# Kernel optimization log

Hardware: AMD Instinct MI355X
Metric: run time of the kernel (lower is better)

The kernel has to match this reference:

```python
import jax, jax.numpy as jnp
import numpy as np

B, N, M, K = 2, 50000, 50000, 16
C_IN, C_ADD, C_MID = 64, 3, 16


def setup_inputs() -> dict:
    key = jax.random.key(0)
    k1, k2, k3, k4 = jax.random.split(key, 4)
    return {
        "input_features": jax.random.normal(k1, (B, N, C_IN), dtype=jnp.float32),
        "neighbor_inds": jax.random.randint(k2, (B, M, K), 0, N, dtype=jnp.int64),
        "weightnet": jax.random.normal(k3, (B, M, K, C_MID), dtype=jnp.float32),
        "additional_features": jax.random.normal(k4, (B, M, K, C_ADD), dtype=jnp.float32),
    }


def reference(input_features, neighbor_inds, weightnet, additional_features):
    # Gather neighbor features: [B, M, K, C_in]
    gathered = jax.vmap(lambda feat, idx: feat[idx])(input_features, neighbor_inds)
    # Concatenate additional per-neighbor features: [B, M, K, C_in + C_add]
    cat = jnp.concatenate([gathered, additional_features], axis=-1)
    # Weighted reduce over neighbors: [B, M, C_total, C_mid]
    out = jnp.einsum("bmkc,bmkw->bmcw", cat, weightnet)
    b, m = out.shape[:2]
    return out.reshape(b, m, -1)
```

## Files before the change

### kernel.cpp

```cpp
#include <hip/hip_runtime.h>
#include <cstdint>
#include <cstddef>


namespace {
constexpr int B_   = 2;
constexpr int N_   = 50000;
constexpr int M_   = 50000;
constexpr int KNB  = 16;
constexpr int CIN  = 64;
constexpr int COUT = 67 * 16;
constexpr int PAIRS = B_ * M_;
constexpr int FELEMS = B_ * N_ * CIN;
}

typedef unsigned int u32;
typedef float  f32x4   __attribute__((ext_vector_type(4)));
typedef short  short8  __attribute__((ext_vector_type(8)));
typedef short  short4v __attribute__((ext_vector_type(4)));
typedef u32    u32x4   __attribute__((ext_vector_type(4)));
typedef u32    u32x2   __attribute__((ext_vector_type(2)));

struct IdxS   { int v[16]; };
struct StageF { float bg[4][8]; float ad[8]; float wf[8]; };

static __device__ __forceinline__ short8 pack_bf8(const float* x) {
  u32x4 w;
  #pragma unroll
  for (int q = 0; q < 4; ++q)
    w[q] = __builtin_amdgcn_perm(__builtin_bit_cast(u32, x[2*q+1]),
                                 __builtin_bit_cast(u32, x[2*q]),
                                 0x07060302u);
  return __builtin_bit_cast(short8, w);
}

static __device__ __forceinline__ short4v pack_bf4(const float* x) {
  u32x2 w;
  #pragma unroll
  for (int q = 0; q < 2; ++q)
    w[q] = __builtin_amdgcn_perm(__builtin_bit_cast(u32, x[2*q+1]),
                                 __builtin_bit_cast(u32, x[2*q]),
                                 0x07060302u);
  return __builtin_bit_cast(short4v, w);
}

static __device__ __forceinline__ u32 bfrne(float x) {
  u32 u = __builtin_bit_cast(u32, x);
  return (u + 0x7FFFu + ((u >> 16) & 1u)) >> 16;
}

__global__ __launch_bounds__(256)
void cvt_feat_bf16(const float* __restrict__ src, unsigned short* __restrict__ dst) {
  const int n4 = FELEMS / 4;
  int i = blockIdx.x * blockDim.x + threadIdx.x;
  const int stride = gridDim.x * blockDim.x;
  const f32x4* s4 = reinterpret_cast<const f32x4*>(src);
  for (; i < n4; i += stride) {
    f32x4 v = s4[i];
    u32x2 w;
    w[0] = bfrne(v[0]) | (bfrne(v[1]) << 16);
    w[1] = bfrne(v[2]) | (bfrne(v[3]) << 16);
    *reinterpret_cast<u32x2*>(dst + 4 * (size_t)i) = w;
  }
}

static __device__ __forceinline__ void load_idx(const int* __restrict__ idxp, IdxS& r) {
  #pragma unroll
  for (int j = 0; j < 16; ++j)
    r.v[j] = __builtin_amdgcn_readfirstlane(idxp[j]);
}

#if __has_builtin(__builtin_amdgcn_mfma_f32_16x16x16bf16_1k)

__global__ __launch_bounds__(256, 8)
void pconv10(const unsigned short* __restrict__ tbl, const int* __restrict__ inds,
             const float* __restrict__ wnet, const float* __restrict__ addf,
             float* __restrict__ out)
{
  const int lane = threadIdx.x & 63;
  const int cc = lane & 15, g = lane >> 4;
  const int g1 = g & 1, g2 = g >> 1;
  const int gw = __builtin_amdgcn_readfirstlane(
      (int)((blockIdx.x * blockDim.x + threadIdx.x) >> 6));
  const int nw = (int)((gridDim.x * blockDim.x) >> 6);
  if (gw >= PAIRS) return;

  IdxS iCur, iNext;
  load_idx(inds + (size_t)gw * KNB, iCur);

  for (int p = gw; p < PAIRS; p += nw) {
    const int pn = (p + nw < PAIRS) ? (p + nw) : gw;
    load_idx(inds + (size_t)pn * KNB, iNext);

    const int b = (p >= M_) ? 1 : 0;
    const unsigned short* __restrict__ fb  = tbl + (size_t)b * N_ * CIN;
    const float* __restrict__ wnp = wnet + (size_t)p * 256;
    const float* __restrict__ adp = addf + (size_t)p * 48;

    int row[4];
    #pragma unroll
    for (int j = 0; j < 4; ++j) {
      const int ra = g1 ? iCur.v[4 + j]  : iCur.v[j];
      const int rb = g1 ? iCur.v[12 + j] : iCur.v[8 + j];
      row[j] = g2 ? rb : ra;
    }

    u32 bg[4][4];
    #pragma unroll
    for (int j = 0; j < 4; ++j) {
      const unsigned short* __restrict__ rp = fb + (((u32)row[j]) << 6) + (u32)cc;
      #pragma unroll
      for (int t = 0; t < 4; ++t)
        bg[t][j] = rp[t * 16];
    }

    float wf[4];
    const float* __restrict__ wp = wnp + g * 64 + cc;
    #pragma unroll
    for (int j = 0; j < 4; ++j)
      wf[j] = __builtin_nontemporal_load(wp + j * 16);

    float ad[4];
    const float* __restrict__ ap = adp + g * 12 + cc;
    #pragma unroll
    for (int j = 0; j < 4; ++j)
      ad[j] = (cc < 3) ? __builtin_nontemporal_load(ap + j * 3) : 0.f;

    const short4v a = pack_bf4(wf);
    float* __restrict__ op = out + (size_t)p * COUT;
    const int soff = cc * 16 + g * 4;

    #pragma unroll
    for (int t = 0; t < 4; ++t) {
      u32x2 w;
      w[0] = bg[t][0] | (bg[t][1] << 16);
      w[1] = bg[t][2] | (bg[t][3] << 16);
      const short4v bb = __builtin_bit_cast(short4v, w);
      f32x4 acc = {0.f, 0.f, 0.f, 0.f};
      acc = __builtin_amdgcn_mfma_f32_16x16x16bf16_1k(a, bb, acc, 0, 0, 0);
      __builtin_nontemporal_store(acc, reinterpret_cast<f32x4*>(op + soff + t * 256));
    }
    {
      const short4v bb = pack_bf4(ad);
      f32x4 acc = {0.f, 0.f, 0.f, 0.f};
      acc = __builtin_amdgcn_mfma_f32_16x16x16bf16_1k(a, bb, acc, 0, 0, 0);
      if (cc < 3)
        __builtin_nontemporal_store(acc, reinterpret_cast<f32x4*>(op + soff + 1024));
    }

    #pragma unroll
    for (int j = 0; j < 16; ++j) iCur.v[j] = iNext.v[j];
  }
}

#else

struct StageT { unsigned short bg[4][8]; float ad[8]; float wf[8]; };

static __device__ __forceinline__ void load_stage_t(const unsigned short* __restrict__ fb,
                                                    const float* __restrict__ wnp,
                                                    const float* __restrict__ adp,
                                                    const IdxS& I, int lane, StageT& S) {
  const int cc = lane & 15;
  if (lane < 32) {
    const int hi = lane >> 4;
    int rows[8];
    #pragma unroll
    for (int j = 0; j < 8; ++j) rows[j] = hi ? I.v[j + 8] : I.v[j];
    #pragma unroll
    for (int j = 0; j < 8; ++j) {
      const u32 rb = ((u32)rows[j]) << 6;
      #pragma unroll
      for (int t = 0; t < 4; ++t)
        S.bg[t][j] = fb[rb + (u32)(t * 16 + cc)];
    }
    const u32 woff = (hi ? 128u : 0u) + (u32)cc;
    #pragma unroll
    for (int j = 0; j < 8; ++j)
      S.wf[j] = __builtin_nontemporal_load(wnp + woff + j * 16);
    if (cc < 3) {
      const u32 aoff = (hi ? 24u : 0u) + (u32)cc;
      #pragma unroll
      for (int j = 0; j < 8; ++j)
        S.ad[j] = __builtin_nontemporal_load(adp + aoff + j * 3);
    }
  }
}

__global__ __launch_bounds__(256, 4)
void pconv10(const unsigned short* __restrict__ tbl, const int* __restrict__ inds,
             const float* __restrict__ wnet, const float* __restrict__ addf,
             float* __restrict__ out)
{
  const int lane = threadIdx.x & 63;
  const int gw = __builtin_amdgcn_readfirstlane(
      (int)((blockIdx.x * blockDim.x + threadIdx.x) >> 6));
  const int nw = (int)((gridDim.x * blockDim.x) >> 6);
  if (gw >= PAIRS) return;

  IdxS iCur, iNext;
  load_idx(inds + (size_t)gw * KNB, iCur);
  for (int p = gw; p < PAIRS; p += nw) {
    const int pn = (p + nw < PAIRS) ? (p + nw) : gw;
    load_idx(inds + (size_t)pn * KNB, iNext);
    const int b = (p >= M_) ? 1 : 0;
    StageT S = {};
    load_stage_t(tbl + (size_t)b * N_ * CIN, wnet + (size_t)p * 256,
                 addf + (size_t)p * 48, iCur, lane, S);
    const int cc = lane & 15, g = lane >> 4;
    const int soff = cc * 16 + g * 4;
    float* op = out + (size_t)p * COUT;
    const short8 a = pack_bf8(S.wf);
    #pragma unroll
    for (int t = 0; t < 4; ++t) {
      short8 bb;
      #pragma unroll
      for (int j = 0; j < 8; ++j) bb[j] = (short)S.bg[t][j];
      f32x4 acc = {0.f, 0.f, 0.f, 0.f};
      acc = __builtin_amdgcn_mfma_f32_16x16x32_bf16(a, bb, acc, 0, 0, 0);
      __builtin_nontemporal_store(acc, reinterpret_cast<f32x4*>(op + soff + t * 256));
    }
    {
      const short8 bb = pack_bf8(S.ad);
      f32x4 acc = {0.f, 0.f, 0.f, 0.f};
      acc = __builtin_amdgcn_mfma_f32_16x16x32_bf16(a, bb, acc, 0, 0, 0);
      if (cc < 3)
        __builtin_nontemporal_store(acc, reinterpret_cast<f32x4*>(op + soff + 1024));
    }
    #pragma unroll
    for (int j = 0; j < 16; ++j) iCur.v[j] = iNext.v[j];
  }
}

#endif

static __device__ __forceinline__ void load_stage_f(const float* __restrict__ fb,
                                                    const float* __restrict__ wnp,
                                                    const float* __restrict__ adp,
                                                    const IdxS& I, int lane, StageF& S) {
  const int cc = lane & 15;
  if (lane < 32) {
    const int hi = lane >> 4;
    int rows[8];
    #pragma unroll
    for (int j = 0; j < 8; ++j) rows[j] = hi ? I.v[j + 8] : I.v[j];
    #pragma unroll
    for (int j = 0; j < 8; ++j) {
      const u32 rb = ((u32)rows[j]) << 6;
      #pragma unroll
      for (int t = 0; t < 4; ++t)
        S.bg[t][j] = fb[rb + (u32)(t * 16 + cc)];
    }
    const u32 woff = (hi ? 128u : 0u) + (u32)cc;
    #pragma unroll
    for (int j = 0; j < 8; ++j)
      S.wf[j] = __builtin_nontemporal_load(wnp + woff + j * 16);
    if (cc < 3) {
      const u32 aoff = (hi ? 24u : 0u) + (u32)cc;
      #pragma unroll
      for (int j = 0; j < 8; ++j)
        S.ad[j] = __builtin_nontemporal_load(adp + aoff + j * 3);
    }
  }
}

__global__ __launch_bounds__(256, 4)
void pconv10_f32(const float* __restrict__ feat, const int* __restrict__ inds,
                 const float* __restrict__ wnet, const float* __restrict__ addf,
                 float* __restrict__ out)
{
  const int lane = threadIdx.x & 63;
  const int gw = __builtin_amdgcn_readfirstlane(
      (int)((blockIdx.x * blockDim.x + threadIdx.x) >> 6));
  const int nw = (int)((gridDim.x * blockDim.x) >> 6);
  if (gw >= PAIRS) return;

  IdxS iCur, iNext;
  load_idx(inds + (size_t)gw * KNB, iCur);
  for (int p = gw; p < PAIRS; p += nw) {
    const int pn = (p + nw < PAIRS) ? (p + nw) : gw;
    load_idx(inds + (size_t)pn * KNB, iNext);
    const int b = (p >= M_) ? 1 : 0;
    StageF S = {};
    load_stage_f(feat + (size_t)b * N_ * CIN, wnet + (size_t)p * 256,
                 addf + (size_t)p * 48, iCur, lane, S);
    const int cc = lane & 15, g = lane >> 4;
    const int soff = cc * 16 + g * 4;
    float* op = out + (size_t)p * COUT;
    const short8 a = pack_bf8(S.wf);
    #pragma unroll
    for (int t = 0; t < 4; ++t) {
      const short8 bb = pack_bf8(S.bg[t]);
      f32x4 acc = {0.f, 0.f, 0.f, 0.f};
      acc = __builtin_amdgcn_mfma_f32_16x16x32_bf16(a, bb, acc, 0, 0, 0);
      __builtin_nontemporal_store(acc, reinterpret_cast<f32x4*>(op + soff + t * 256));
    }
    {
      const short8 bb = pack_bf8(S.ad);
      f32x4 acc = {0.f, 0.f, 0.f, 0.f};
      acc = __builtin_amdgcn_mfma_f32_16x16x32_bf16(a, bb, acc, 0, 0, 0);
      if (cc < 3)
        __builtin_nontemporal_store(acc, reinterpret_cast<f32x4*>(op + soff + 1024));
    }
    #pragma unroll
    for (int j = 0; j < 16; ++j) iCur.v[j] = iNext.v[j];
  }
}

extern "C" void kernel_launch(void* const* d_in, const int* in_sizes, int n_in,
                              void* d_out, int out_size, void* d_ws, size_t ws_size,
                              hipStream_t stream) {
  const float* feat = (const float*)d_in[0];
  const int*   inds = (const int*)d_in[1];
  const float* wnet = (const float*)d_in[2];
  const float* addf = (const float*)d_in[3];
  float* outp = (float*)d_out;

  const size_t TBL_BYTES = (size_t)FELEMS * sizeof(unsigned short);

  dim3 grid(4096), block(256);
  if (ws_size >= TBL_BYTES) {
    unsigned short* tbl = (unsigned short*)d_ws;
    hipLaunchKernelGGL(cvt_feat_bf16, dim3(2048), dim3(256), 0, stream, feat, tbl);
    hipLaunchKernelGGL(pconv10, grid, block, 0, stream, tbl, inds, wnet, addf, outp);
  } else {
    hipLaunchKernelGGL(pconv10_f32, grid, block, 0, stream,
                       feat, inds, wnet, addf, outp);
  }
}
```

Before: 166.1 us.

## Software-pipeline gathers three pairs deep with rotating register stages

Restructures the MFMA path so each wave keeps three rotating stage buffers: the gathered feature rows, weightnet and additional loads for pair p+2 are issued while pair p is computed and stored, and the indices for p+3 are prefetched. The aim is to hide gather latency behind compute by keeping more memory requests in flight per wave. The cost is higher register use, so launch bounds drop from 8 to 4 waves per SIMD, which reduces occupancy. The loop is unrolled three times with a break in each copy.

```diff
diff --git a/kernel.cpp b/kernel.cpp
--- a/kernel.cpp
+++ b/kernel.cpp
@@ -22,6 +22,7 @@
 typedef u32    u32x2   __attribute__((ext_vector_type(2)));
 
 struct IdxS   { int v[16]; };
+struct StageG { u32 bg[4][4]; float wf[4]; float ad[4]; };
 struct StageF { float bg[4][8]; float ad[8]; float wf[8]; };
 
 static __device__ __forceinline__ short8 pack_bf8(const float* x) {
@@ -72,8 +73,67 @@
 
 #if __has_builtin(__builtin_amdgcn_mfma_f32_16x16x16bf16_1k)
 
-__global__ __launch_bounds__(256, 8)
-void pconv10(const unsigned short* __restrict__ tbl, const int* __restrict__ inds,
+static __device__ __forceinline__ void issue_loads(const unsigned short* __restrict__ tbl,
+                                                   const float* __restrict__ wnet,
+                                                   const float* __restrict__ addf,
+                                                   int q, const IdxS& I,
+                                                   int cc, int g1, int g2, int g,
+                                                   StageG& S) {
+  const unsigned short* __restrict__ fb =
+      tbl + ((q >= M_) ? (size_t)N_ * CIN : 0);
+  const float* __restrict__ wnp = wnet + (size_t)q * 256;
+  const float* __restrict__ adp = addf + (size_t)q * 48;
+
+  int row[4];
+  #pragma unroll
+  for (int j = 0; j < 4; ++j) {
+    const int ra = g1 ? I.v[4 + j]  : I.v[j];
+    const int rb = g1 ? I.v[12 + j] : I.v[8 + j];
+    row[j] = g2 ? rb : ra;
+  }
+  #pragma unroll
+  for (int j = 0; j < 4; ++j) {
+    const unsigned short* __restrict__ rp = fb + (((u32)row[j]) << 6) + (u32)cc;
+    #pragma unroll
+    for (int t = 0; t < 4; ++t)
+      S.bg[t][j] = rp[t * 16];
+  }
+  const float* __restrict__ wp = wnp + g * 64 + cc;
+  #pragma unroll
+  for (int j = 0; j < 4; ++j)
+    S.wf[j] = __builtin_nontemporal_load(wp + j * 16);
+  const float* __restrict__ ap = adp + g * 12 + cc;
+  #pragma unroll
+  for (int j = 0; j < 4; ++j)
+    S.ad[j] = (cc < 3) ? __builtin_nontemporal_load(ap + j * 3) : 0.f;
+}
+
+static __device__ __forceinline__ void compute_store(const StageG& S,
+                                                     float* __restrict__ op,
+                                                     int cc, int g) {
+  const int soff = cc * 16 + g * 4;
+  const short4v a = pack_bf4(S.wf);
+  #pragma unroll
+  for (int t = 0; t < 4; ++t) {
+    u32x2 w;
+    w[0] = S.bg[t][0] | (S.bg[t][1] << 16);
+    w[1] = S.bg[t][2] | (S.bg[t][3] << 16);
+    const short4v bb = __builtin_bit_cast(short4v, w);
+    f32x4 acc = {0.f, 0.f, 0.f, 0.f};
+    acc = __builtin_amdgcn_mfma_f32_16x16x16bf16_1k(a, bb, acc, 0, 0, 0);
+    __builtin_nontemporal_store(acc, reinterpret_cast<f32x4*>(op + soff + t * 256));
+  }
+  {
+    const short4v bb = pack_bf4(S.ad);
+    f32x4 acc = {0.f, 0.f, 0.f, 0.f};
+    acc = __builtin_amdgcn_mfma_f32_16x16x16bf16_1k(a, bb, acc, 0, 0, 0);
+    if (cc < 3)
+      __builtin_nontemporal_store(acc, reinterpret_cast<f32x4*>(op + soff + 1024));
+  }
+}
+
+__global__ __launch_bounds__(256, 4)
+void pconv11(const unsigned short* __restrict__ tbl, const int* __restrict__ inds,
              const float* __restrict__ wnet, const float* __restrict__ addf,
              float* __restrict__ out)
 {
@@ -85,71 +145,44 @@
   const int nw = (int)((gridDim.x * blockDim.x) >> 6);
   if (gw >= PAIRS) return;
 
-  IdxS iCur, iNext;
-  load_idx(inds + (size_t)gw * KNB, iCur);
-
-  for (int p = gw; p < PAIRS; p += nw) {
-    const int pn = (p + nw < PAIRS) ? (p + nw) : gw;
-    load_idx(inds + (size_t)pn * KNB, iNext);
-
-    const int b = (p >= M_) ? 1 : 0;
-    const unsigned short* __restrict__ fb  = tbl + (size_t)b * N_ * CIN;
-    const float* __restrict__ wnp = wnet + (size_t)p * 256;
-    const float* __restrict__ adp = addf + (size_t)p * 48;
-
-    int row[4];
-    #pragma unroll
-    for (int j = 0; j < 4; ++j) {
-      const int ra = g1 ? iCur.v[4 + j]  : iCur.v[j];
-      const int rb = g1 ? iCur.v[12 + j] : iCur.v[8 + j];
-      row[j] = g2 ? rb : ra;
-    }
-
-    u32 bg[4][4];
-    #pragma unroll
-    for (int j = 0; j < 4; ++j) {
-      const unsigned short* __restrict__ rp = fb + (((u32)row[j]) << 6) + (u32)cc;
-      #pragma unroll
-      for (int t = 0; t < 4; ++t)
-        bg[t][j] = rp[t * 16];
-    }
-
-    float wf[4];
-    const float* __restrict__ wp = wnp + g * 64 + cc;
-    #pragma unroll
-    for (int j = 0; j < 4; ++j)
-      wf[j] = __builtin_nontemporal_load(wp + j * 16);
-
-    float ad[4];
-    const float* __restrict__ ap = adp + g * 12 + cc;
-    #pragma unroll
-    for (int j = 0; j < 4; ++j)
-      ad[j] = (cc < 3) ? __builtin_nontemporal_load(ap + j * 3) : 0.f;
-
-    const short4v a = pack_bf4(wf);
-    float* __restrict__ op = out + (size_t)p * COUT;
-    const int soff = cc * 16 + g * 4;
-
-    #pragma unroll
-    for (int t = 0; t < 4; ++t) {
-      u32x2 w;
-      w[0] = bg[t][0] | (bg[t][1] << 16);
-      w[1] = bg[t][2] | (bg[t][3] << 16);
-      const short4v bb = __builtin_bit_cast(short4v, w);
-      f32x4 acc = {0.f, 0.f, 0.f, 0.f};
-      acc = __builtin_amdgcn_mfma_f32_16x16x16bf16_1k(a, bb, acc, 0, 0, 0);
-      __builtin_nontemporal_store(acc, reinterpret_cast<f32x4*>(op + soff + t * 256));
-    }
-    {
-      const short4v bb = pack_bf4(ad);
-      f32x4 acc = {0.f, 0.f, 0.f, 0.f};
-      acc = __builtin_amdgcn_mfma_f32_16x16x16bf16_1k(a, bb, acc, 0, 0, 0);
-      if (cc < 3)
-        __builtin_nontemporal_store(acc, reinterpret_cast<f32x4*>(op + soff + 1024));
-    }
-
-    #pragma unroll
-    for (int j = 0; j < 16; ++j) iCur.v[j] = iNext.v[j];
+  IdxS iA, iB, iC;
+  StageG sA, sB, sC;
+  int p = gw;
+
+  load_idx(inds + (size_t)p * KNB, iA);
+  { const int q = (p + nw < PAIRS) ? (p + nw) : gw;
+    load_idx(inds + (size_t)q * KNB, iB); }
+  { const int q = (p + 2 * nw < PAIRS) ? (p + 2 * nw) : gw;
+    load_idx(inds + (size_t)q * KNB, iC); }
+  issue_loads(tbl, wnet, addf, p, iA, cc, g1, g2, g, sA);
+  { const int q = (p + nw < PAIRS) ? (p + nw) : gw;
+    issue_loads(tbl, wnet, addf, q, iB, cc, g1, g2, g, sB); }
+
+  while (true) {
+    {
+      const int q2 = (p + 2 * nw < PAIRS) ? (p + 2 * nw) : gw;
+      issue_loads(tbl, wnet, addf, q2, iC, cc, g1, g2, g, sC);
+      const int q3 = (p + 3 * nw < PAIRS) ? (p + 3 * nw) : gw;
+      load_idx(inds + (size_t)q3 * KNB, iA);
+      compute_store(sA, out + (size_t)p * COUT, cc, g);
+      p += nw; if (p >= PAIRS) break;
+    }
+    {
+      const int q2 = (p + 2 * nw < PAIRS) ? (p + 2 * nw) : gw;
+      issue_loads(tbl, wnet, addf, q2, iA, cc, g1, g2, g, sA);
+      const int q3 = (p + 3 * nw < PAIRS) ? (p + 3 * nw) : gw;
+      load_idx(inds + (size_t)q3 * KNB, iB);
+      compute_store(sB, out + (size_t)p * COUT, cc, g);
+      p += nw; if (p >= PAIRS) break;
+    }
+    {
+      const int q2 = (p + 2 * nw < PAIRS) ? (p + 2 * nw) : gw;
+      issue_loads(tbl, wnet, addf, q2, iB, cc, g1, g2, g, sB);
+      const int q3 = (p + 3 * nw < PAIRS) ? (p + 3 * nw) : gw;
+      load_idx(inds + (size_t)q3 * KNB, iC);
+      compute_store(sC, out + (size_t)p * COUT, cc, g);
+      p += nw; if (p >= PAIRS) break;
+    }
   }
 }
 
@@ -188,7 +221,7 @@
 }
 
 __global__ __launch_bounds__(256, 4)
-void pconv10(const unsigned short* __restrict__ tbl, const int* __restrict__ inds,
+void pconv11(const unsigned short* __restrict__ tbl, const int* __restrict__ inds,
              const float* __restrict__ wnet, const float* __restrict__ addf,
              float* __restrict__ out)
 {
@@ -265,7 +298,7 @@
 }
 
 __global__ __launch_bounds__(256, 4)
-void pconv10_f32(const float* __restrict__ feat, const int* __restrict__ inds,
+void pconv11_f32(const float* __restrict__ feat, const int* __restrict__ inds,
                  const float* __restrict__ wnet, const float* __restrict__ addf,
                  float* __restrict__ out)
 {
@@ -322,9 +355,9 @@
   if (ws_size >= TBL_BYTES) {
     unsigned short* tbl = (unsigned short*)d_ws;
     hipLaunchKernelGGL(cvt_feat_bf16, dim3(2048), dim3(256), 0, stream, feat, tbl);
-    hipLaunchKernelGGL(pconv10, grid, block, 0, stream, tbl, inds, wnet, addf, outp);
+    hipLaunchKernelGGL(pconv11, grid, block, 0, stream, tbl, inds, wnet, addf, outp);
   } else {
-    hipLaunchKernelGGL(pconv10_f32, grid, block, 0, stream,
+    hipLaunchKernelGGL(pconv11_f32, grid, block, 0, stream,
                        feat, inds, wnet, addf, outp);
   }
 }
```

New measurement: 158.6 us. 1.05x faster.

## Pipeline gathers three pairs deep with vectorized row loads staged through LDS

Applied to the files above, without the earlier changes.

Replaces the per-pair gather kernel with a software-pipelined loop that keeps three pairs in flight. Neighbor rows are fetched as 16-byte vector loads by lane (one row per 4 lanes) instead of scalar 2-byte loads, then transposed through a padded per-wave LDS tile before feeding the MFMA. Index loads are per-lane rather than readfirstlane scalar loads, and the grid shrinks from 4096 to 1024 blocks with launch bounds lowered to 4 waves per SIMD. The aim is to hide gather latency and cut load instruction count, at the cost of higher register pressure, LDS traffic and fewer resident waves.

```diff
diff --git a/kernel.cpp b/kernel.cpp
--- a/kernel.cpp
+++ b/kernel.cpp
@@ -12,6 +12,7 @@
 constexpr int COUT = 67 * 16;
 constexpr int PAIRS = B_ * M_;
 constexpr int FELEMS = B_ * N_ * CIN;
+constexpr int LROW = 72;
 }
 
 typedef unsigned int u32;
@@ -21,8 +22,8 @@
 typedef u32    u32x4   __attribute__((ext_vector_type(4)));
 typedef u32    u32x2   __attribute__((ext_vector_type(2)));
 
+struct StageF { float bg[4][8]; float ad[8]; float wf[8]; };
 struct IdxS   { int v[16]; };
-struct StageF { float bg[4][8]; float ad[8]; float wf[8]; };
 
 static __device__ __forceinline__ short8 pack_bf8(const float* x) {
   u32x4 w;
@@ -64,98 +65,131 @@
   }
 }
 
-static __device__ __forceinline__ void load_idx(const int* __restrict__ idxp, IdxS& r) {
-  #pragma unroll
-  for (int j = 0; j < 16; ++j)
-    r.v[j] = __builtin_amdgcn_readfirstlane(idxp[j]);
-}
-
 #if __has_builtin(__builtin_amdgcn_mfma_f32_16x16x16bf16_1k)
 
-__global__ __launch_bounds__(256, 8)
-void pconv10(const unsigned short* __restrict__ tbl, const int* __restrict__ inds,
+__global__ __launch_bounds__(256, 4)
+void pconv13(const unsigned short* __restrict__ tbl, const int* __restrict__ inds,
              const float* __restrict__ wnet, const float* __restrict__ addf,
              float* __restrict__ out)
 {
+  __shared__ alignas(16) unsigned short sg[4][16 * LROW];
   const int lane = threadIdx.x & 63;
+  const int wid  = threadIdx.x >> 6;
+  unsigned short* __restrict__ lds = &sg[wid][0];
   const int cc = lane & 15, g = lane >> 4;
-  const int g1 = g & 1, g2 = g >> 1;
+  const int r_ = lane >> 2, s_ = lane & 3;
   const int gw = __builtin_amdgcn_readfirstlane(
       (int)((blockIdx.x * blockDim.x + threadIdx.x) >> 6));
   const int nw = (int)((gridDim.x * blockDim.x) >> 6);
   if (gw >= PAIRS) return;
 
-  IdxS iCur, iNext;
-  load_idx(inds + (size_t)gw * KNB, iCur);
-
-  for (int p = gw; p < PAIRS; p += nw) {
-    const int pn = (p + nw < PAIRS) ? (p + nw) : gw;
-    load_idx(inds + (size_t)pn * KNB, iNext);
-
-    const int b = (p >= M_) ? 1 : 0;
-    const unsigned short* __restrict__ fb  = tbl + (size_t)b * N_ * CIN;
-    const float* __restrict__ wnp = wnet + (size_t)p * 256;
-    const float* __restrict__ adp = addf + (size_t)p * 48;
-
-    int row[4];
-    #pragma unroll
-    for (int j = 0; j < 4; ++j) {
-      const int ra = g1 ? iCur.v[4 + j]  : iCur.v[j];
-      const int rb = g1 ? iCur.v[12 + j] : iCur.v[8 + j];
-      row[j] = g2 ? rb : ra;
-    }
-
-    u32 bg[4][4];
-    #pragma unroll
-    for (int j = 0; j < 4; ++j) {
-      const unsigned short* __restrict__ rp = fb + (((u32)row[j]) << 6) + (u32)cc;
-      #pragma unroll
-      for (int t = 0; t < 4; ++t)
-        bg[t][j] = rp[t * 16];
-    }
-
-    float wf[4];
-    const float* __restrict__ wp = wnp + g * 64 + cc;
-    #pragma unroll
-    for (int j = 0; j < 4; ++j)
-      wf[j] = __builtin_nontemporal_load(wp + j * 16);
-
-    float ad[4];
-    const float* __restrict__ ap = adp + g * 12 + cc;
-    #pragma unroll
-    for (int j = 0; j < 4; ++j)
-      ad[j] = (cc < 3) ? __builtin_nontemporal_load(ap + j * 3) : 0.f;
-
-    const short4v a = pack_bf4(wf);
-    float* __restrict__ op = out + (size_t)p * COUT;
-    const int soff = cc * 16 + g * 4;
-
-    #pragma unroll
-    for (int t = 0; t < 4; ++t) {
-      u32x2 w;
-      w[0] = bg[t][0] | (bg[t][1] << 16);
-      w[1] = bg[t][2] | (bg[t][3] << 16);
-      const short4v bb = __builtin_bit_cast(short4v, w);
-      f32x4 acc = {0.f, 0.f, 0.f, 0.f};
-      acc = __builtin_amdgcn_mfma_f32_16x16x16bf16_1k(a, bb, acc, 0, 0, 0);
-      __builtin_nontemporal_store(acc, reinterpret_cast<f32x4*>(op + soff + t * 256));
-    }
-    {
-      const short4v bb = pack_bf4(ad);
-      f32x4 acc = {0.f, 0.f, 0.f, 0.f};
-      acc = __builtin_amdgcn_mfma_f32_16x16x16bf16_1k(a, bb, acc, 0, 0, 0);
-      if (cc < 3)
-        __builtin_nontemporal_store(acc, reinterpret_cast<f32x4*>(op + soff + 1024));
-    }
-
-    #pragma unroll
-    for (int j = 0; j < 16; ++j) iCur.v[j] = iNext.v[j];
-  }
+#define CLQ(x) (((x) < PAIRS) ? (x) : gw)
+
+  int   row0, row1, row2;
+  u32x4 ga0, gb0, ga1, gb1, ga2, gb2;
+  float wf0[4], wf1[4], wf2[4], ad0[4], ad1[4], ad2[4];
+
+#define ROWL(R, q) do { const int _q = CLQ(q); \
+      R = inds[(size_t)_q * KNB + r_]; } while (0)
+
+#define GATH(Sa, Sb, R, q) do { const int _q = CLQ(q); \
+      const unsigned short* __restrict__ _fb = tbl + ((_q >= M_) ? (size_t)N_ * CIN : 0) \
+          + (((u32)(R)) << 6) + (u32)(s_ * 8); \
+      Sa = *reinterpret_cast<const u32x4*>(_fb); \
+      Sb = *reinterpret_cast<const u32x4*>(_fb + 32); } while (0)
+
+#define STRM(WF, AD, q) do { const int _q = CLQ(q); \
+      const float* __restrict__ _wp = wnet + (size_t)_q * 256 + g * 64 + cc; \
+      WF[0] = __builtin_nontemporal_load(_wp); \
+      WF[1] = __builtin_nontemporal_load(_wp + 16); \
+      WF[2] = __builtin_nontemporal_load(_wp + 32); \
+      WF[3] = __builtin_nontemporal_load(_wp + 48); \
+      const float* __restrict__ _ap = addf + (size_t)_q * 48 + g * 12 + cc; \
+      AD[0] = (cc < 3) ? __builtin_nontemporal_load(_ap)     : 0.f; \
+      AD[1] = (cc < 3) ? __builtin_nontemporal_load(_ap + 3) : 0.f; \
+      AD[2] = (cc < 3) ? __builtin_nontemporal_load(_ap + 6) : 0.f; \
+      AD[3] = (cc < 3) ? __builtin_nontemporal_load(_ap + 9) : 0.f; } while (0)
+
+#define WRIT(Sa, Sb) do { \
+      *reinterpret_cast<u32x4*>(lds + r_ * LROW + s_ * 8)      = Sa; \
+      *reinterpret_cast<u32x4*>(lds + r_ * LROW + s_ * 8 + 32) = Sb; } while (0)
+
+#define COMP(WF, AD, pp) do { \
+      float* __restrict__ _op = out + (size_t)(pp) * COUT; \
+      const short4v _a = pack_bf4(WF); \
+      const int _soff = cc * 16 + g * 4; \
+      _Pragma("unroll") \
+      for (int t = 0; t < 4; ++t) { \
+        const int _cb = t * 16 + cc; \
+        const u32 _e0 = lds[(4 * g + 0) * LROW + _cb]; \
+        const u32 _e1 = lds[(4 * g + 1) * LROW + _cb]; \
+        const u32 _e2 = lds[(4 * g + 2) * LROW + _cb]; \
+        const u32 _e3 = lds[(4 * g + 3) * LROW + _cb]; \
+        u32x2 _w; _w[0] = _e0 | (_e1 << 16); _w[1] = _e2 | (_e3 << 16); \
+        const short4v _bb = __builtin_bit_cast(short4v, _w); \
+        f32x4 _acc = {0.f, 0.f, 0.f, 0.f}; \
+        _acc = __builtin_amdgcn_mfma_f32_16x16x16bf16_1k(_a, _bb, _acc, 0, 0, 0); \
+        __builtin_nontemporal_store(_acc, reinterpret_cast<f32x4*>(_op + _soff + t * 256)); \
+      } \
+      { const short4v _bb = pack_bf4(AD); \
+        f32x4 _acc = {0.f, 0.f, 0.f, 0.f}; \
+        _acc = __builtin_amdgcn_mfma_f32_16x16x16bf16_1k(_a, _bb, _acc, 0, 0, 0); \
+        if (cc < 3) \
+          __builtin_nontemporal_store(_acc, reinterpret_cast<f32x4*>(_op + _soff + 1024)); \
+      } } while (0)
+
+  int p = gw;
+  ROWL(row0, p); ROWL(row1, p + nw); ROWL(row2, p + 2 * nw);
+  GATH(ga0, gb0, row0, p);
+  GATH(ga1, gb1, row1, p + nw);
+  ROWL(row0, p + 3 * nw);
+  STRM(wf0, ad0, p);
+  STRM(wf1, ad1, p + nw);
+
+  while (true) {
+    {
+      ROWL(row1, p + 4 * nw);
+      GATH(ga2, gb2, row2, p + 2 * nw);
+      STRM(wf2, ad2, p + 2 * nw);
+      WRIT(ga0, gb0);
+      COMP(wf0, ad0, p);
+      p += nw; if (p >= PAIRS) break;
+    }
+    {
+      ROWL(row2, p + 4 * nw);
+      GATH(ga0, gb0, row0, p + 2 * nw);
+      STRM(wf0, ad0, p + 2 * nw);
+      WRIT(ga1, gb1);
+      COMP(wf1, ad1, p);
+      p += nw; if (p >= PAIRS) break;
+    }
+    {
+      ROWL(row0, p + 4 * nw);
+      GATH(ga1, gb1, row1, p + 2 * nw);
+      STRM(wf1, ad1, p + 2 * nw);
+      WRIT(ga2, gb2);
+      COMP(wf2, ad2, p);
+      p += nw; if (p >= PAIRS) break;
+    }
+  }
+
+#undef CLQ
+#undef ROWL
+#undef GATH
+#undef STRM
+#undef WRIT
+#undef COMP
 }
 
 #else
 
 struct StageT { unsigned short bg[4][8]; float ad[8]; float wf[8]; };
+
+static __device__ __forceinline__ void load_idx_s(const int* __restrict__ idxp, IdxS& r) {
+  #pragma unroll
+  for (int j = 0; j < 16; ++j)
+    r.v[j] = __builtin_amdgcn_readfirstlane(idxp[j]);
+}
 
 static __device__ __forceinline__ void load_stage_t(const unsigned short* __restrict__ fb,
                                                     const float* __restrict__ wnp,
@@ -188,7 +222,7 @@
 }
 
 __global__ __launch_bounds__(256, 4)
-void pconv10(const unsigned short* __restrict__ tbl, const int* __restrict__ inds,
+void pconv13(const unsigned short* __restrict__ tbl, const int* __restrict__ inds,
              const float* __restrict__ wnet, const float* __restrict__ addf,
              float* __restrict__ out)
 {
@@ -199,10 +233,10 @@
   if (gw >= PAIRS) return;
 
   IdxS iCur, iNext;
-  load_idx(inds + (size_t)gw * KNB, iCur);
+  load_idx_s(inds + (size_t)gw * KNB, iCur);
   for (int p = gw; p < PAIRS; p += nw) {
     const int pn = (p + nw < PAIRS) ? (p + nw) : gw;
-    load_idx(inds + (size_t)pn * KNB, iNext);
+    load_idx_s(inds + (size_t)pn * KNB, iNext);
     const int b = (p >= M_) ? 1 : 0;
     StageT S = {};
     load_stage_t(tbl + (size_t)b * N_ * CIN, wnet + (size_t)p * 256,
@@ -234,6 +268,12 @@
 
 #endif
 
+static __device__ __forceinline__ void load_idx_f(const int* __restrict__ idxp, IdxS& r) {
+  #pragma unroll
+  for (int j = 0; j < 16; ++j)
+    r.v[j] = __builtin_amdgcn_readfirstlane(idxp[j]);
+}
+
 static __device__ __forceinline__ void load_stage_f(const float* __restrict__ fb,
                                                     const float* __restrict__ wnp,
                                                     const float* __restrict__ adp,
@@ -265,7 +305,7 @@
 }
 
 __global__ __launch_bounds__(256, 4)
-void pconv10_f32(const float* __restrict__ feat, const int* __restrict__ inds,
+void pconv13_f32(const float* __restrict__ feat, const int* __restrict__ inds,
                  const float* __restrict__ wnet, const float* __restrict__ addf,
                  float* __restrict__ out)
 {
@@ -276,10 +316,10 @@
   if (gw >= PAIRS) return;
 
   IdxS iCur, iNext;
-  load_idx(inds + (size_t)gw * KNB, iCur);
+  load_idx_f(inds + (size_t)gw * KNB, iCur);
   for (int p = gw; p < PAIRS; p += nw) {
     const int pn = (p + nw < PAIRS) ? (p + nw) : gw;
-    load_idx(inds + (size_t)pn * KNB, iNext);
+    load_idx_f(inds + (size_t)pn * KNB, iNext);
     const int b = (p >= M_) ? 1 : 0;
     StageF S = {};
     load_stage_f(feat + (size_t)b * N_ * CIN, wnet + (size_t)p * 256,
@@ -318,13 +358,13 @@
 
   const size_t TBL_BYTES = (size_t)FELEMS * sizeof(unsigned short);
 
-  dim3 grid(4096), block(256);
+  dim3 grid(1024), block(256);
   if (ws_size >= TBL_BYTES) {
     unsigned short* tbl = (unsigned short*)d_ws;
     hipLaunchKernelGGL(cvt_feat_bf16, dim3(2048), dim3(256), 0, stream, feat, tbl);
-    hipLaunchKernelGGL(pconv10, grid, block, 0, stream, tbl, inds, wnet, addf, outp);
+    hipLaunchKernelGGL(pconv13, grid, block, 0, stream, tbl, inds, wnet, addf, outp);
   } else {
-    hipLaunchKernelGGL(pconv10_f32, grid, block, 0, stream,
+    hipLaunchKernelGGL(pconv13_f32, grid, block, 0, stream,
                        feat, inds, wnet, addf, outp);
   }
 }
```

New measurement: 155.9 us. -6.1%, faster.
